# Performance work log

Hardware: AMD Instinct MI355X
Metric: run time of the kernel (lower is better)

The kernel has to match this reference:

```python
import jax, jax.numpy as jnp
import numpy as np

NUM_CLASSES = 1000
FEAT_DIM = 256
N = 262144
ALPHA = 0.5


def setup_inputs() -> dict:
    key = jax.random.key(0)
    k1, k2, k3 = jax.random.split(key, 3)
    features = jax.random.normal(k1, (N, FEAT_DIM), dtype=jnp.float32)
    labels = jax.random.randint(k2, (N,), 0, NUM_CLASSES, dtype=jnp.int64)
    centers = jax.random.normal(k3, (NUM_CLASSES, FEAT_DIM), dtype=jnp.float32)
    return {"features": features, "labels": labels, "centers": centers}


def reference(features, labels, centers):
    # Fused segment-mean: scatter-add of features + per-class counts,
    # replacing the per-class python loop in the original.
    sums = jax.ops.segment_sum(features, labels, num_segments=NUM_CLASSES)  # [C, D]
    counts = jax.ops.segment_sum(
        jnp.ones((features.shape[0],), dtype=features.dtype),
        labels,
        num_segments=NUM_CLASSES,
    )  # [C]
    has_samples = counts > 0
    safe_counts = jnp.where(has_samples, counts, 1.0)
    class_means = sums / safe_counts[:, None]  # [C, D]
    # EMA update only for classes present in the batch.
    updated = (1.0 - ALPHA) * centers + ALPHA * class_means
    new_centers = jnp.where(has_samples[:, None], updated, centers)
    return new_centers
```

## Files before the change

kernel.cpp:

```cpp
#include <hip/hip_runtime.h>

constexpr int N    = 262144;
constexpr int C    = 1000;
constexpr int D4   = 64;
constexpr int CPAD = 1024;
constexpr int NB   = 64;
constexpr int ROWS_PER_B = N / NB;
constexpr float ALPHA = 0.5f;

typedef float vfloat4 __attribute__((ext_vector_type(4)));


__global__ __launch_bounds__(256) void hist_kernel(
        const int* __restrict__ labels, int* __restrict__ hist) {
    __shared__ int h[CPAD];
    int t = threadIdx.x;
    for (int i = t; i < CPAD; i += 256) h[i] = 0;
    __syncthreads();
    int base = blockIdx.x * ROWS_PER_B;
    for (int i = t; i < ROWS_PER_B; i += 256)
        atomicAdd(&h[labels[base + i]], 1);
    __syncthreads();
    int* out = hist + blockIdx.x * CPAD;
    for (int i = t; i < CPAD; i += 256) out[i] = h[i];
}

__global__ __launch_bounds__(1024) void scan_kernel(
        const int* __restrict__ hist,
        int* __restrict__ counts,
        int* __restrict__ offs,
        int* __restrict__ blockcursor) {
    __shared__ int s[CPAD];
    int t = threadIdx.x;
    int total = 0;
    #pragma unroll 8
    for (int b = 0; b < NB; ++b) total += hist[b * CPAD + t];
    counts[t] = total;
    s[t] = total;
    __syncthreads();
    for (int off = 1; off < CPAD; off <<= 1) {
        int add = (t >= off) ? s[t - off] : 0;
        __syncthreads();
        s[t] += add;
        __syncthreads();
    }
    int run = s[t] - total;
    offs[t] = run;
    for (int b = 0; b < NB; ++b) {
        blockcursor[b * CPAD + t] = run;
        run += hist[b * CPAD + t];
    }
}

__global__ __launch_bounds__(256) void scatter_kernel(
        const int* __restrict__ labels,
        const int* __restrict__ blockcursor,
        int* __restrict__ rowidx) {
    __shared__ int cur[CPAD];
    int t = threadIdx.x;
    const int* bc = blockcursor + blockIdx.x * CPAD;
    for (int i = t; i < CPAD; i += 256) cur[i] = bc[i];
    __syncthreads();
    int base = blockIdx.x * ROWS_PER_B;
    for (int i = t; i < ROWS_PER_B; i += 256) {
        int row = base + i;
        int pos = atomicAdd(&cur[labels[row]], 1);
        rowidx[pos] = row;
    }
}

__global__ __launch_bounds__(256) void class_reduce_kernel(
        const vfloat4* __restrict__ feat4,
        const float4* __restrict__ cen4,
        const int* __restrict__ offs,
        const int* __restrict__ counts,
        const int* __restrict__ rowidx,
        float4* __restrict__ out4) {
    int c     = blockIdx.x;
    int start = offs[c];
    int cnt   = counts[c];
    int wave  = threadIdx.x >> 6;
    int lane  = threadIdx.x & 63;
    int end   = start + cnt;

    vfloat4 acc[8];
    #pragma unroll
    for (int u = 0; u < 8; ++u) acc[u] = (vfloat4)0.f;

    int j = start + wave;
    for (; j + 28 < end; j += 32) {
        int r[8];
        #pragma unroll
        for (int u = 0; u < 8; ++u) r[u] = rowidx[j + 4 * u];
        #pragma unroll
        for (int u = 0; u < 8; ++u) {
            vfloat4 v = __builtin_nontemporal_load(&feat4[(long)r[u] * D4 + lane]);
            acc[u] += v;
        }
    }
    for (; j < end; j += 4) {
        int r = rowidx[j];
        vfloat4 v = __builtin_nontemporal_load(&feat4[(long)r * D4 + lane]);
        acc[0] += v;
    }
    #pragma unroll
    for (int u = 1; u < 8; ++u) acc[0] += acc[u];

    __shared__ float red[4][64][4];
    red[wave][lane][0] = acc[0].x;
    red[wave][lane][1] = acc[0].y;
    red[wave][lane][2] = acc[0].z;
    red[wave][lane][3] = acc[0].w;
    __syncthreads();

    if (wave == 0) {
        float sx = red[0][lane][0] + red[1][lane][0] + red[2][lane][0] + red[3][lane][0];
        float sy = red[0][lane][1] + red[1][lane][1] + red[2][lane][1] + red[3][lane][1];
        float sz = red[0][lane][2] + red[1][lane][2] + red[2][lane][2] + red[3][lane][2];
        float sw = red[0][lane][3] + red[1][lane][3] + red[2][lane][3] + red[3][lane][3];

        float4 cen = cen4[c * D4 + lane];
        float4 o;
        if (cnt > 0) {
            float s = ALPHA / (float)cnt;
            o.x = (1.0f - ALPHA) * cen.x + sx * s;
            o.y = (1.0f - ALPHA) * cen.y + sy * s;
            o.z = (1.0f - ALPHA) * cen.z + sz * s;
            o.w = (1.0f - ALPHA) * cen.w + sw * s;
        } else {
            o = cen;
        }
        out4[c * D4 + lane] = o;
    }
}

extern "C" void kernel_launch(void* const* d_in, const int* in_sizes, int n_in,
                              void* d_out, int out_size, void* d_ws, size_t ws_size,
                              hipStream_t stream) {
    const vfloat4* feat4  = (const vfloat4*)d_in[0];
    const int*     labels = (const int*)d_in[1];
    const float4*  cen4   = (const float4*)d_in[2];
    float4*        out4   = (float4*)d_out;

    int* hist        = (int*)d_ws;
    int* counts      = hist + NB * CPAD;
    int* offs        = counts + CPAD;
    int* blockcursor = offs + CPAD;
    int* rowidx      = blockcursor + NB * CPAD;

    hist_kernel<<<NB, 256, 0, stream>>>(labels, hist);
    scan_kernel<<<1, CPAD, 0, stream>>>(hist, counts, offs, blockcursor);
    scatter_kernel<<<NB, 256, 0, stream>>>(labels, blockcursor, rowidx);
    class_reduce_kernel<<<C, 256, 0, stream>>>(feat4, cen4, offs, counts, rowidx, out4);
}
```

Before: 363.2 us.

## Replace per-class block reduction with even segmented reduction plus atomics

The one-block-per-class reduction is replaced by a segmented reduction over the sorted row list. Each wave takes a fixed 64-entry chunk and flushes partial sums to a global sums buffer with float atomics whenever the label changes. A separate EMA kernel then applies the center update. This is meant to fix load imbalance and the low parallelism of 1000 blocks over 262k rows, at the cost of an extra kernel, zeroing the sums buffer, and atomic traffic that makes the float summation order nondeterministic.

```diff
diff --git a/kernel.cpp b/kernel.cpp
--- a/kernel.cpp
+++ b/kernel.cpp
@@ -2,6 +2,7 @@
 
 constexpr int N    = 262144;
 constexpr int C    = 1000;
+constexpr int D    = 256;
 constexpr int D4   = 64;
 constexpr int CPAD = 1024;
 constexpr int NB   = 64;
@@ -12,10 +13,13 @@
 
 
 __global__ __launch_bounds__(256) void hist_kernel(
-        const int* __restrict__ labels, int* __restrict__ hist) {
+        const int* __restrict__ labels, int* __restrict__ hist,
+        float4* __restrict__ sums4) {
     __shared__ int h[CPAD];
     int t = threadIdx.x;
     for (int i = t; i < CPAD; i += 256) h[i] = 0;
+    for (int i = blockIdx.x * 256 + t; i < C * D / 4; i += NB * 256)
+        sums4[i] = float4{0.f, 0.f, 0.f, 0.f};
     __syncthreads();
     int base = blockIdx.x * ROWS_PER_B;
     for (int i = t; i < ROWS_PER_B; i += 256)
@@ -28,7 +32,6 @@
 __global__ __launch_bounds__(1024) void scan_kernel(
         const int* __restrict__ hist,
         int* __restrict__ counts,
-        int* __restrict__ offs,
         int* __restrict__ blockcursor) {
     __shared__ int s[CPAD];
     int t = threadIdx.x;
@@ -45,7 +48,7 @@
         __syncthreads();
     }
     int run = s[t] - total;
-    offs[t] = run;
+    #pragma unroll 4
     for (int b = 0; b < NB; ++b) {
         blockcursor[b * CPAD + t] = run;
         run += hist[b * CPAD + t];
@@ -55,7 +58,7 @@
 __global__ __launch_bounds__(256) void scatter_kernel(
         const int* __restrict__ labels,
         const int* __restrict__ blockcursor,
-        int* __restrict__ rowidx) {
+        int* __restrict__ S) {
     __shared__ int cur[CPAD];
     int t = threadIdx.x;
     const int* bc = blockcursor + blockIdx.x * CPAD;
@@ -64,74 +67,87 @@
     int base = blockIdx.x * ROWS_PER_B;
     for (int i = t; i < ROWS_PER_B; i += 256) {
         int row = base + i;
-        int pos = atomicAdd(&cur[labels[row]], 1);
-        rowidx[pos] = row;
+        int lab = labels[row];
+        int pos = atomicAdd(&cur[lab], 1);
+        S[pos] = (row << 10) | lab;
     }
 }
 
-__global__ __launch_bounds__(256) void class_reduce_kernel(
+__global__ __launch_bounds__(256) void seg_reduce_kernel(
         const vfloat4* __restrict__ feat4,
-        const float4* __restrict__ cen4,
-        const int* __restrict__ offs,
-        const int* __restrict__ counts,
-        const int* __restrict__ rowidx,
-        float4* __restrict__ out4) {
-    int c     = blockIdx.x;
-    int start = offs[c];
-    int cnt   = counts[c];
-    int wave  = threadIdx.x >> 6;
-    int lane  = threadIdx.x & 63;
-    int end   = start + cnt;
+        const int* __restrict__ S,
+        float* __restrict__ sums) {
+    int wave = threadIdx.x >> 6;
+    int lane = threadIdx.x & 63;
+    int base = (blockIdx.x * 4 + wave) * 64;
+    int packed = S[base + lane];
 
-    vfloat4 acc[8];
+    vfloat4 acc = (vfloat4)0.f;
+    int cur = __shfl(packed, 0) & 1023;
+
+    constexpr int PF = 8;
+    int pk[PF];
+    vfloat4 v[PF];
     #pragma unroll
-    for (int u = 0; u < 8; ++u) acc[u] = (vfloat4)0.f;
-
-    int j = start + wave;
-    for (; j + 28 < end; j += 32) {
-        int r[8];
-        #pragma unroll
-        for (int u = 0; u < 8; ++u) r[u] = rowidx[j + 4 * u];
-        #pragma unroll
-        for (int u = 0; u < 8; ++u) {
-            vfloat4 v = __builtin_nontemporal_load(&feat4[(long)r[u] * D4 + lane]);
-            acc[u] += v;
-        }
-    }
-    for (; j < end; j += 4) {
-        int r = rowidx[j];
-        vfloat4 v = __builtin_nontemporal_load(&feat4[(long)r * D4 + lane]);
-        acc[0] += v;
+    for (int j = 0; j < PF; ++j) {
+        pk[j] = __shfl(packed, j);
+        v[j]  = __builtin_nontemporal_load(&feat4[(long)(pk[j] >> 10) * D4 + lane]);
     }
     #pragma unroll
-    for (int u = 1; u < 8; ++u) acc[0] += acc[u];
+    for (int i = 0; i < 64; i += PF) {
+        int npk[PF];
+        vfloat4 nv[PF];
+        if (i + PF < 64) {
+            #pragma unroll
+            for (int j = 0; j < PF; ++j) {
+                npk[j] = __shfl(packed, i + PF + j);
+                nv[j]  = __builtin_nontemporal_load(&feat4[(long)(npk[j] >> 10) * D4 + lane]);
+            }
+        }
+        #pragma unroll
+        for (int j = 0; j < PF; ++j) {
+            int lab = pk[j] & 1023;
+            if (lab != cur) {
+                float* dst = sums + cur * D + lane * 4;
+                unsafeAtomicAdd(dst + 0, acc.x);
+                unsafeAtomicAdd(dst + 1, acc.y);
+                unsafeAtomicAdd(dst + 2, acc.z);
+                unsafeAtomicAdd(dst + 3, acc.w);
+                acc = (vfloat4)0.f;
+                cur = lab;
+            }
+            acc += v[j];
+        }
+        #pragma unroll
+        for (int j = 0; j < PF; ++j) { pk[j] = npk[j]; v[j] = nv[j]; }
+    }
+    float* dst = sums + cur * D + lane * 4;
+    unsafeAtomicAdd(dst + 0, acc.x);
+    unsafeAtomicAdd(dst + 1, acc.y);
+    unsafeAtomicAdd(dst + 2, acc.z);
+    unsafeAtomicAdd(dst + 3, acc.w);
+}
 
-    __shared__ float red[4][64][4];
-    red[wave][lane][0] = acc[0].x;
-    red[wave][lane][1] = acc[0].y;
-    red[wave][lane][2] = acc[0].z;
-    red[wave][lane][3] = acc[0].w;
-    __syncthreads();
-
-    if (wave == 0) {
-        float sx = red[0][lane][0] + red[1][lane][0] + red[2][lane][0] + red[3][lane][0];
-        float sy = red[0][lane][1] + red[1][lane][1] + red[2][lane][1] + red[3][lane][1];
-        float sz = red[0][lane][2] + red[1][lane][2] + red[2][lane][2] + red[3][lane][2];
-        float sw = red[0][lane][3] + red[1][lane][3] + red[2][lane][3] + red[3][lane][3];
-
-        float4 cen = cen4[c * D4 + lane];
-        float4 o;
-        if (cnt > 0) {
-            float s = ALPHA / (float)cnt;
-            o.x = (1.0f - ALPHA) * cen.x + sx * s;
-            o.y = (1.0f - ALPHA) * cen.y + sy * s;
-            o.z = (1.0f - ALPHA) * cen.z + sz * s;
-            o.w = (1.0f - ALPHA) * cen.w + sw * s;
-        } else {
-            o = cen;
-        }
-        out4[c * D4 + lane] = o;
+__global__ __launch_bounds__(256) void ema_kernel(
+        const float4* __restrict__ cen4,
+        const float* __restrict__ sums,
+        const int* __restrict__ counts,
+        float4* __restrict__ out4) {
+    int idx = blockIdx.x * 256 + threadIdx.x;
+    if (idx >= C * D4) return;
+    int c = idx >> 6;
+    int cnt = counts[c];
+    float4 cen = cen4[idx];
+    float4 o = cen;
+    if (cnt > 0) {
+        const float* sp = sums + c * D + (idx & 63) * 4;
+        float s = ALPHA / (float)cnt;
+        o.x = (1.0f - ALPHA) * cen.x + sp[0] * s;
+        o.y = (1.0f - ALPHA) * cen.y + sp[1] * s;
+        o.z = (1.0f - ALPHA) * cen.z + sp[2] * s;
+        o.w = (1.0f - ALPHA) * cen.w + sp[3] * s;
     }
+    out4[idx] = o;
 }
 
 extern "C" void kernel_launch(void* const* d_in, const int* in_sizes, int n_in,
@@ -142,14 +158,15 @@
     const float4*  cen4   = (const float4*)d_in[2];
     float4*        out4   = (float4*)d_out;
 
-    int* hist        = (int*)d_ws;
-    int* counts      = hist + NB * CPAD;
-    int* offs        = counts + CPAD;
-    int* blockcursor = offs + CPAD;
-    int* rowidx      = blockcursor + NB * CPAD;
+    int*   hist        = (int*)d_ws;
+    int*   counts      = hist + NB * CPAD;
+    int*   blockcursor = counts + CPAD;
+    int*   S           = blockcursor + NB * CPAD;
+    float* sums        = (float*)(S + N);
 
-    hist_kernel<<<NB, 256, 0, stream>>>(labels, hist);
-    scan_kernel<<<1, CPAD, 0, stream>>>(hist, counts, offs, blockcursor);
-    scatter_kernel<<<NB, 256, 0, stream>>>(labels, blockcursor, rowidx);
-    class_reduce_kernel<<<C, 256, 0, stream>>>(feat4, cen4, offs, counts, rowidx, out4);
+    hist_kernel<<<NB, 256, 0, stream>>>(labels, hist, (float4*)sums);
+    scan_kernel<<<1, CPAD, 0, stream>>>(hist, counts, blockcursor);
+    scatter_kernel<<<NB, 256, 0, stream>>>(labels, blockcursor, S);
+    seg_reduce_kernel<<<N / 256, 256, 0, stream>>>(feat4, S, sums);
+    ema_kernel<<<(C * D4 + 255) / 256, 256, 0, stream>>>(cen4, sums, counts, out4);
 }
```

After: 367.2 us. Within noise of the previous version (+1.1%).
